# Performance work log

Measured on AMD Instinct MI355X. Metric: run time of the kernel, lower is better.

## Reference

```python
import jax, jax.numpy as jnp
import numpy as np

B, T, C = 2, 1024, 384
H, D = 4, 96            # heads, head_dim
BLK, NG = 16, 24        # HBS block size, num groups (NG*BLK == C)
SQ, PADM = 20, 400      # monarch grid dim, padded monarch dim
E, K, FF = 8, 2, 1536   # experts, top_k, expert hidden
EPS_LN = 1e-5


def _ln(x, g, b):
    m = jnp.mean(x, -1, keepdims=True)
    v = jnp.var(x, -1, keepdims=True)
    return (x - m) * jax.lax.rsqrt(v + EPS_LN) * g + b


def _hbs(x, pre_g, pre_b, blocks, wrow, wcol, alpha, bias):
    """HierarchicalBlockShuffleLayer: block mixing + flip + monarch, fp32."""
    orig = x.shape
    flat = _ln(x, pre_g, pre_b).astype(jnp.float32).reshape(-1, C)
    # block mixing: per-group 16x16 matmuls
    grouped = flat.reshape(-1, NG, BLK)
    y = jnp.einsum('ngb,gbc->ngc', grouped, blocks).reshape(-1, C)
    block_out = y[:, ::-1]  # torch.flip(dims=[-1])
    # monarch: pad to 400, view as 20x20 grid, left/right mix
    grid = jnp.pad(flat, ((0, 0), (0, PADM - C))).reshape(-1, SQ, SQ)
    z = jnp.einsum('nij,jk,lk->nil', grid, wcol, wrow)  # (x @ W_col) @ W_row.T
    mon = z.reshape(-1, PADM)[:, :C]
    out = block_out + alpha * mon + bias
    return out.reshape(orig)


def _rotary(t_len, d):
    inv = 1.0 / (10000.0 ** (jnp.arange(0, d, 2, dtype=jnp.float32) / d))
    fr = jnp.outer(jnp.arange(t_len, dtype=jnp.float32), inv)  # [T, d/2]
    emb = jnp.concatenate([fr, fr], -1)                        # [T, d]
    return jnp.cos(emb), jnp.sin(emb)


def _rotate_half(x):
    x1, x2 = x[..., : x.shape[-1] // 2], x[..., x.shape[-1] // 2:]
    return jnp.concatenate([-x2, x1], -1)


def _attention(xn, qkv_w, qkv_b, proj_pre_g, proj_pre_b, proj_blocks,
               proj_wrow, proj_wcol, proj_alpha, proj_bias,
               attn_norm_g, attn_norm_b, out_norm_g, out_norm_b, focus_gate):
    qkv = xn @ qkv_w + qkv_b  # [B,T,3C]
    q, k, v = jnp.split(qkv, 3, axis=-1)
    q = q.reshape(B, T, H, D).transpose(0, 2, 1, 3)  # bhtd
    k = k.reshape(B, T, H, D).transpose(0, 2, 1, 3)
    v = v.reshape(B, T, H, D).transpose(0, 2, 1, 3)
    cos, sin = _rotary(T, D)
    cos, sin = cos[None, None], sin[None, None]
    q = q * cos + _rotate_half(q) * sin
    k = k * cos + _rotate_half(k) * sin
    scale = 1.0 / jnp.sqrt(jnp.float32(D))
    # ---- linear attention branch (fp32, cumsum recurrence) ----
    Qp = jax.nn.elu(q * scale) + 1.0
    Kp = jax.nn.elu(k * scale) + 1.0
    KV = Kp[..., :, None] * v[..., None, :]          # bhtde
    KVc = jnp.cumsum(KV, axis=2)
    Kc = jnp.cumsum(Kp, axis=2)
    num = jnp.einsum('bhtd,bhtde->bhte', Qp, KVc)
    den = jnp.einsum('bhtd,bhtd->bht', Qp, Kc)[..., None]
    y_lin = num / (den + 1e-4)
    y_lin = _ln(y_lin, attn_norm_g, attn_norm_b)     # LN over head_dim
    # ---- sharp causal SDPA branch ----
    scores = jnp.einsum('bhtd,bhsd->bhts', q, k) * scale
    mask = jnp.tril(jnp.ones((T, T), dtype=bool))
    scores = jnp.where(mask, scores, -jnp.inf)
    y_sharp = jnp.einsum('bhts,bhsd->bhtd', jax.nn.softmax(scores, -1), v)
    # ---- gated combine ----
    a = jax.nn.sigmoid(focus_gate)
    y = a * y_sharp + (1.0 - a) * y_lin
    y = y.transpose(0, 2, 1, 3).reshape(B, T, C)
    y = _ln(y, out_norm_g, out_norm_b)
    return _hbs(y, proj_pre_g, proj_pre_b, proj_blocks, proj_wrow, proj_wcol,
                proj_alpha, proj_bias)


def _moe(xn, gate_w, w1, b1, w2, b2):
    xf = xn.reshape(-1, C)  # [N,C]
    logits = jnp.clip(xf @ gate_w, -20.0, 20.0)
    w, idx = jax.lax.top_k(logits, K)
    w = jax.nn.softmax(w, -1)
    # dense per-token expert weights [N,E] (same math as sparse dispatch, eval mode)
    wfull = jnp.sum(jax.nn.one_hot(idx, E, dtype=xf.dtype) * w[..., None], axis=1)
    h = jax.nn.gelu(jnp.einsum('nc,ech->neh', xf, w1) + b1, approximate=False)
    o = jnp.einsum('neh,ehc->nec', h, w2) + b2
    out = jnp.einsum('nec,ne->nc', o, wfull)
    return out.reshape(B, T, C)


def setup_inputs() -> dict:
    key = jax.random.key(0)
    ks = jax.random.split(key, 10)
    s = 0.02
    return {
        'x': jax.random.normal(ks[0], (B, T, C), jnp.float32),
        'ln1_g': jnp.ones((C,), jnp.float32), 'ln1_b': jnp.zeros((C,), jnp.float32),
        'ln2_g': jnp.ones((C,), jnp.float32), 'ln2_b': jnp.zeros((C,), jnp.float32),
        'qkv_w': jax.random.normal(ks[1], (C, 3 * C), jnp.float32) * s,
        'qkv_b': jnp.zeros((3 * C,), jnp.float32),
        'proj_pre_g': jnp.ones((C,), jnp.float32), 'proj_pre_b': jnp.zeros((C,), jnp.float32),
        'proj_blocks': jax.random.normal(ks[2], (NG, BLK, BLK), jnp.float32) * 0.125,
        'proj_wrow': jax.random.normal(ks[3], (SQ, SQ), jnp.float32) * 0.05,
        'proj_wcol': jax.random.normal(ks[4], (SQ, SQ), jnp.float32) * 0.05,
        'proj_alpha': jnp.zeros((), jnp.float32),
        'proj_bias': jnp.zeros((C,), jnp.float32),
        'attn_norm_g': jnp.ones((D,), jnp.float32), 'attn_norm_b': jnp.zeros((D,), jnp.float32),
        'out_norm_g': jnp.ones((C,), jnp.float32), 'out_norm_b': jnp.zeros((C,), jnp.float32),
        'focus_gate': jnp.zeros((), jnp.float32),
        'gate_w': jax.random.normal(ks[5], (C, E), jnp.float32) * s,
        'moe_w1': jax.random.normal(ks[6], (E, C, FF), jnp.float32) * s,
        'moe_b1': jnp.zeros((E, FF), jnp.float32),
        'moe_w2': jax.random.normal(ks[7], (E, FF, C), jnp.float32) * s,
        'moe_b2': jnp.zeros((E, C), jnp.float32),
    }


def reference(x, ln1_g, ln1_b, ln2_g, ln2_b, qkv_w, qkv_b,
              proj_pre_g, proj_pre_b, proj_blocks, proj_wrow, proj_wcol,
              proj_alpha, proj_bias, attn_norm_g, attn_norm_b,
              out_norm_g, out_norm_b, focus_gate, gate_w,
              moe_w1, moe_b1, moe_w2, moe_b2):
    h = x + _attention(_ln(x, ln1_g, ln1_b), qkv_w, qkv_b, proj_pre_g, proj_pre_b,
                       proj_blocks, proj_wrow, proj_wcol, proj_alpha, proj_bias,
                       attn_norm_g, attn_norm_b, out_norm_g, out_norm_b, focus_gate)
    out = h + _moe(_ln(h, ln2_g, ln2_b), gate_w, moe_w1, moe_b1, moe_w2, moe_b2)
    return out
```

## Files before the change

kernel.cpp:

```cpp
#include <hip/hip_runtime.h>
#include <math.h>

#define BB 2
#define TT 1024
#define CC 384
#define HH 4
#define DD 96
#define EE 8
#define FFD 1536
#define NROW (BB*TT)
#define QKVN (3*CC)
#define NSLOT (NROW*2)

typedef float f32x4 __attribute__((ext_vector_type(4)));
typedef short bf16x8 __attribute__((ext_vector_type(8)));

__device__ __forceinline__ float wredSum64(float v) {
#pragma unroll
  for (int o = 32; o > 0; o >>= 1) v += __shfl_xor(v, o, 64);
  return v;
}
__device__ __forceinline__ float rsum16(float v) {
#pragma unroll
  for (int o = 8; o > 0; o >>= 1) v += __shfl_xor(v, o, 16);
  return v;
}
__device__ __forceinline__ float rmax16(float v) {
#pragma unroll
  for (int o = 8; o > 0; o >>= 1) v = fmaxf(v, __shfl_xor(v, o, 16));
  return v;
}
__device__ __forceinline__ float dot4f(const float4 a, const float4 b) {
  return a.x*b.x + a.y*b.y + a.z*b.z + a.w*b.w;
}
__device__ __forceinline__ float blockRed128(float v, float* red) {
  v = wredSum64(v);
  const int w = threadIdx.x >> 6;
  if ((threadIdx.x & 63) == 0) red[w] = v;
  __syncthreads();
  float r = red[0] + red[1];
  __syncthreads();
  return r;
}
__device__ __forceinline__ float elup1(float x) {
  return x > 0.f ? x + 1.f : expf(x);
}
__device__ __forceinline__ unsigned short f2bf(float f) {
  unsigned int u = __float_as_uint(f);
  u = (u + 0x7FFFu + ((u >> 16) & 1u)) >> 16;
  return (unsigned short)u;
}

__global__ void zero_counts_kernel(int* counts) {
  if (threadIdx.x < EE) counts[threadIdx.x] = 0;
}

__global__ __launch_bounds__(256) void transconv_kernel(
    const float* __restrict__ src, unsigned short* __restrict__ dst,
    int K, int N) {
  src += (size_t)blockIdx.z * K * N;
  dst += (size_t)blockIdx.z * K * N;
  const int k0 = blockIdx.y * 32, n0 = blockIdx.x * 32;
  __shared__ float tile[32][33];
  const int t = threadIdx.x;
  const int ki = t >> 3, nj = (t & 7) * 4;
  const float4 v = *(const float4*)&src[(size_t)(k0 + ki) * N + n0 + nj];
  tile[ki][nj] = v.x; tile[ki][nj + 1] = v.y;
  tile[ki][nj + 2] = v.z; tile[ki][nj + 3] = v.w;
  __syncthreads();
  const int ni = t >> 3, kj = (t & 7) * 4;
  ushort4 o;
  o.x = f2bf(tile[kj][ni]);     o.y = f2bf(tile[kj + 1][ni]);
  o.z = f2bf(tile[kj + 2][ni]); o.w = f2bf(tile[kj + 3][ni]);
  *(ushort4*)&dst[(size_t)(n0 + ni) * K + k0 + kj] = o;
}

__global__ __launch_bounds__(64) void ln_row_kernel(
    const float* __restrict__ xin, const float* __restrict__ g,
    const float* __restrict__ b, float* __restrict__ xout) {
  const int row = blockIdx.x;
  const int lane = threadIdx.x;
  const size_t base = (size_t)row * CC;
  float v[6];
#pragma unroll
  for (int p = 0; p < 6; ++p) v[p] = xin[base + lane + 64 * p];
  float s = v[0] + v[1] + v[2] + v[3] + v[4] + v[5];
  s = wredSum64(s);
  const float mu = s * (1.f / CC);
  float sq = 0.f;
#pragma unroll
  for (int p = 0; p < 6; ++p) { float d = v[p] - mu; sq += d * d; }
  sq = wredSum64(sq);
  const float rinv = rsqrtf(sq * (1.f / CC) + 1e-5f);
#pragma unroll
  for (int p = 0; p < 6; ++p) {
    const int c = lane + 64 * p;
    xout[base + c] = (v[p] - mu) * rinv * g[c] + b[c];
  }
}

__global__ __launch_bounds__(256) void gemm_qkv_kernel(
    const float* __restrict__ A, const float* __restrict__ Bw,
    const float* __restrict__ bias, float* __restrict__ Cout) {
  const int N = QKVN, K = CC;
  const int n0 = blockIdx.x * 64, m0 = blockIdx.y * 64;
  __shared__ float As[16][68];
  __shared__ float Bs[16][64];
  const int tid = threadIdx.x, tx = tid & 15, ty = tid >> 4;
  const int akk = tid & 15, am = tid >> 4;
  const int bn = tid & 63, bk = tid >> 6;
  float acc[4][4] = {};
  for (int k0 = 0; k0 < K; k0 += 16) {
#pragma unroll
    for (int q = 0; q < 4; ++q) {
      As[akk][am + 16 * q] = A[(size_t)(m0 + am + 16 * q) * K + k0 + akk];
      Bs[bk + 4 * q][bn] = Bw[(size_t)(k0 + bk + 4 * q) * N + n0 + bn];
    }
    __syncthreads();
#pragma unroll
    for (int kk = 0; kk < 16; ++kk) {
      const float4 av = *(const float4*)&As[kk][ty * 4];
      const float4 bv = *(const float4*)&Bs[kk][tx * 4];
      const float aa[4] = {av.x, av.y, av.z, av.w};
      const float bb4[4] = {bv.x, bv.y, bv.z, bv.w};
#pragma unroll
      for (int i = 0; i < 4; ++i)
#pragma unroll
        for (int jj = 0; jj < 4; ++jj) acc[i][jj] += aa[i] * bb4[jj];
    }
    __syncthreads();
  }
#pragma unroll
  for (int i = 0; i < 4; ++i) {
    const int r = m0 + ty * 4 + i;
#pragma unroll
    for (int jj = 0; jj < 4; ++jj) {
      const int c = n0 + tx * 4 + jj;
      Cout[(size_t)r * N + c] = acc[i][jj] + bias[c];
    }
  }
}

__global__ __launch_bounds__(256) void rope_kernel(
    const float* __restrict__ qkv, float* __restrict__ qr, float* __restrict__ kr,
    float* __restrict__ qp, float* __restrict__ kp) {
  const int gid = blockIdx.x * 256 + threadIdx.x;
  const int i = gid % 48;
  const int t = (gid / 48) % TT;
  const int h = (gid / (48 * TT)) % HH;
  const int b = gid / (48 * TT * HH);
  const float inv = 1.0f / powf(10000.0f, (float)i * (1.0f / 48.0f));
  const float ang = (float)t * inv;
  float sn, cs;
  sincosf(ang, &sn, &cs);
  const float* row = qkv + ((size_t)(b * TT + t)) * QKVN + h * DD;
  const float q1 = row[i], q2 = row[i + 48];
  const float k1 = row[CC + i], k2 = row[CC + i + 48];
  const float qo1 = q1 * cs - q2 * sn, qo2 = q2 * cs + q1 * sn;
  const float ko1 = k1 * cs - k2 * sn, ko2 = k2 * cs + k1 * sn;
  const size_t ob = ((size_t)((b * HH + h) * TT + t)) * DD;
  qr[ob + i] = qo1; qr[ob + i + 48] = qo2;
  kr[ob + i] = ko1; kr[ob + i + 48] = ko2;
  const float scale = 0.10206207261596577f;
  qp[ob + i] = elup1(qo1 * scale); qp[ob + i + 48] = elup1(qo2 * scale);
  kp[ob + i] = elup1(ko1 * scale); kp[ob + i + 48] = elup1(ko2 * scale);
}

__global__ __launch_bounds__(256, 2) void attn_kernel(
    const float* __restrict__ qr, const float* __restrict__ kr,
    const float* __restrict__ qp, const float* __restrict__ kp,
    const float* __restrict__ qkv, const float* __restrict__ ang,
    const float* __restrict__ anb, const float* __restrict__ fgp,
    float* __restrict__ y_attn) {
  __shared__ float Qt[16][100];
  __shared__ float Qpt[16][100];
  __shared__ float Kt[32][100];
  __shared__ float Kpt[32][100];
  __shared__ float Vt[32][100];
  __shared__ float Ps[16][34];
  __shared__ float Pl[16][34];
  const int idx = blockIdx.x;
  const int qt = 63 - (idx >> 3);
  const int bh = idx & 7, b = bh >> 2, h = bh & 3;
  const int tid = threadIdx.x, j = tid & 15, rg = tid >> 4;
  const float a = 1.f / (1.f + expf(-fgp[0]));
  const int t0 = qt << 4;
  const int t = t0 + rg;
  const size_t qbase = ((size_t)bh * TT + t0) * DD;
#pragma unroll
  for (int p = 0; p < 6; ++p) {
    const int i = tid + 256 * p, r = i / 96, d = i - r * 96;
    Qt[r][d] = qr[qbase + i];
    Qpt[r][d] = qp[qbase + i];
  }
  float accS[6] = {}, accN[6] = {};
  float mrow = -1e30f, lrow = 0.f, den = 0.f;
  const int nc = (qt >> 1) + 1;
  __syncthreads();
  for (int c = 0; c < nc; ++c) {
    const int s0 = c << 5;
    const float* vb = qkv + ((size_t)(b * TT + s0)) * QKVN + 2 * CC + h * DD;
    const size_t kb = ((size_t)bh * TT + s0) * DD;
#pragma unroll
    for (int p = 0; p < 12; ++p) {
      const int i = tid + 256 * p, s = i / 96, d = i - s * 96;
      Kt[s][d] = kr[kb + i];
      Kpt[s][d] = kp[kb + i];
      Vt[s][d] = vb[(size_t)s * QKVN + d];
    }
    __syncthreads();
    float ds0 = 0.f, ds1 = 0.f, dl0 = 0.f, dl1 = 0.f;
#pragma unroll
    for (int dd = 0; dd < 96; dd += 4) {
      const float4 qa = *(const float4*)&Qt[rg][dd];
      const float4 ka = *(const float4*)&Kt[j][dd];
      const float4 k2 = *(const float4*)&Kt[j + 16][dd];
      ds0 += dot4f(qa, ka); ds1 += dot4f(qa, k2);
      const float4 pa = *(const float4*)&Qpt[rg][dd];
      const float4 fa = *(const float4*)&Kpt[j][dd];
      const float4 f2 = *(const float4*)&Kpt[j + 16][dd];
      dl0 += dot4f(pa, fa); dl1 += dot4f(pa, f2);
    }
    const float scale = 0.10206207261596577f;
    float sc0 = ds0 * scale, sc1 = ds1 * scale;
    if (c == nc - 1) {
      if (s0 + j > t)      { sc0 = -1e30f; dl0 = 0.f; }
      if (s0 + j + 16 > t) { sc1 = -1e30f; dl1 = 0.f; }
    }
    const float cm = rmax16(fmaxf(sc0, sc1));
    const float mn = fmaxf(mrow, cm);
    const float sf = expf(mrow - mn);
    const float p0 = expf(sc0 - mn), p1 = expf(sc1 - mn);
    lrow = lrow * sf + rsum16(p0 + p1);
    mrow = mn;
    den += rsum16(dl0 + dl1);
#pragma unroll
    for (int u = 0; u < 6; ++u) accS[u] *= sf;
    Ps[rg][j] = p0; Ps[rg][j + 16] = p1;
    Pl[rg][j] = dl0; Pl[rg][j + 16] = dl1;
    __syncthreads();
    const int c0 = j * 6;
#pragma unroll
    for (int s = 0; s < 32; s += 2) {
      const float2 pA = *(const float2*)&Ps[rg][s];
      const float2 lA = *(const float2*)&Pl[rg][s];
      const float* v0p = &Vt[s][c0];
      const float* v1p = v0p + 100;
      float va[6], vb2[6];
      *(float2*)&va[0] = *(const float2*)(v0p);
      *(float2*)&va[2] = *(const float2*)(v0p + 2);
      *(float2*)&va[4] = *(const float2*)(v0p + 4);
      *(float2*)&vb2[0] = *(const float2*)(v1p);
      *(float2*)&vb2[2] = *(const float2*)(v1p + 2);
      *(float2*)&vb2[4] = *(const float2*)(v1p + 4);
#pragma unroll
      for (int u = 0; u < 6; ++u) {
        accS[u] += pA.x * va[u] + pA.y * vb2[u];
        accN[u] += lA.x * va[u] + lA.y * vb2[u];
      }
    }
    __syncthreads();
  }
  const float invl = 1.0f / lrow;
  const float dinv = 1.0f / (den + 1e-4f);
  float yl[6];
  float s1 = 0.f;
#pragma unroll
  for (int u = 0; u < 6; ++u) { yl[u] = accN[u] * dinv; s1 += yl[u]; }
  s1 = rsum16(s1);
  const float mu = s1 * (1.f / DD);
  float s2 = 0.f;
#pragma unroll
  for (int u = 0; u < 6; ++u) { const float d = yl[u] - mu; s2 += d * d; }
  s2 = rsum16(s2);
  const float rr = rsqrtf(s2 * (1.f / DD) + 1e-5f);
  const size_t ob = ((size_t)(b * TT + t)) * CC + h * DD + j * 6;
#pragma unroll
  for (int u = 0; u < 6; ++u) {
    const float ylin = (yl[u] - mu) * rr * ang[j * 6 + u] + anb[j * 6 + u];
    const float ys = accS[u] * invl;
    y_attn[ob + u] = a * ys + (1.f - a) * ylin;
  }
}

__global__ __launch_bounds__(128) void hbs_kernel(
    const float* __restrict__ y_attn, const float* __restrict__ x,
    const float* __restrict__ outg, const float* __restrict__ outb,
    const float* __restrict__ preg, const float* __restrict__ preb,
    const float* __restrict__ blocks, const float* __restrict__ wrow,
    const float* __restrict__ wcol, const float* __restrict__ alphap,
    const float* __restrict__ biasv, const float* __restrict__ ln2g,
    const float* __restrict__ ln2b, const float* __restrict__ gatew,
    float* __restrict__ hout, unsigned short* __restrict__ xn2,
    int* __restrict__ tok_idx, float* __restrict__ tok_w, int* __restrict__ counts) {
  __shared__ float flatS[CC];
  __shared__ float ybuf[CC];
  __shared__ float xbuf[CC];
  __shared__ float tmp[400];
  __shared__ float red[2];
  __shared__ float logit[EE];
  const int row = blockIdx.x, tid = threadIdx.x;
  const size_t base = (size_t)row * CC;
  float v[3];
#pragma unroll
  for (int p = 0; p < 3; ++p) v[p] = y_attn[base + tid + 128 * p];
  float s = blockRed128(v[0] + v[1] + v[2], red);
  float mu = s * (1.f / CC);
  float sq = 0.f;
#pragma unroll
  for (int p = 0; p < 3; ++p) { const float d = v[p] - mu; sq += d * d; }
  sq = blockRed128(sq, red);
  float rin = rsqrtf(sq * (1.f / CC) + 1e-5f);
  float w[3];
#pragma unroll
  for (int p = 0; p < 3; ++p) {
    const int c = tid + 128 * p;
    w[p] = (v[p] - mu) * rin * outg[c] + outb[c];
  }
  s = blockRed128(w[0] + w[1] + w[2], red);
  mu = s * (1.f / CC);
  sq = 0.f;
#pragma unroll
  for (int p = 0; p < 3; ++p) { const float d = w[p] - mu; sq += d * d; }
  sq = blockRed128(sq, red);
  rin = rsqrtf(sq * (1.f / CC) + 1e-5f);
#pragma unroll
  for (int p = 0; p < 3; ++p) {
    const int c = tid + 128 * p;
    flatS[c] = (w[p] - mu) * rin * preg[c] + preb[c];
  }
  __syncthreads();
#pragma unroll
  for (int p = 0; p < 3; ++p) {
    const int o = tid + 128 * p;
    const int g = o >> 4, cc = o & 15;
    const float* bp = blocks + g * 256 + cc;
    const float* fp = flatS + g * 16;
    float acc = 0.f;
#pragma unroll
    for (int bb = 0; bb < 16; ++bb) acc += fp[bb] * bp[bb * 16];
    ybuf[o] = acc;
  }
#pragma unroll
  for (int p = 0; p < 4; ++p) {
    const int o = tid + 128 * p;
    if (o < 400) {
      const int i = o / 20, k = o - i * 20;
      float acc = 0.f;
#pragma unroll
      for (int jj = 0; jj < 20; ++jj) {
        const int src = i * 20 + jj;
        const float gv = (src < CC) ? flatS[src] : 0.f;
        acc += gv * wcol[jj * 20 + k];
      }
      tmp[o] = acc;
    }
  }
  __syncthreads();
  const float alpha = alphap[0];
  float hr[3];
#pragma unroll
  for (int p = 0; p < 3; ++p) {
    const int o = tid + 128 * p;
    const int i = o / 20, ll = o - i * 20;
    float mon = 0.f;
#pragma unroll
    for (int k = 0; k < 20; ++k) mon += tmp[i * 20 + k] * wrow[ll * 20 + k];
    const float hb = ybuf[383 - o] + alpha * mon + biasv[o];
    const float hv = x[base + o] + hb;
    hout[base + o] = hv;
    hr[p] = hv;
  }
  s = blockRed128(hr[0] + hr[1] + hr[2], red);
  mu = s * (1.f / CC);
  sq = 0.f;
#pragma unroll
  for (int p = 0; p < 3; ++p) { const float d = hr[p] - mu; sq += d * d; }
  sq = blockRed128(sq, red);
  rin = rsqrtf(sq * (1.f / CC) + 1e-5f);
#pragma unroll
  for (int p = 0; p < 3; ++p) {
    const int c = tid + 128 * p;
    const float xv = (hr[p] - mu) * rin * ln2g[c] + ln2b[c];
    xn2[base + c] = f2bf(xv);
    xbuf[c] = xv;
  }
  __syncthreads();
  const int e = tid >> 4, jj = tid & 15;
  float part = 0.f;
  for (int c = jj; c < CC; c += 16) part += xbuf[c] * gatew[c * EE + e];
  part = rsum16(part);
  if (jj == 0) logit[e] = fminf(20.f, fmaxf(-20.f, part));
  __syncthreads();
  if (tid == 0) {
    float lg[EE];
#pragma unroll
    for (int ee = 0; ee < EE; ++ee) lg[ee] = logit[ee];
    int i0 = 0; float v0 = lg[0];
#pragma unroll
    for (int ee = 1; ee < EE; ++ee) if (lg[ee] > v0) { v0 = lg[ee]; i0 = ee; }
    int i1 = -1; float v1 = -1e30f;
#pragma unroll
    for (int ee = 0; ee < EE; ++ee)
      if (ee != i0 && lg[ee] > v1) { v1 = lg[ee]; i1 = ee; }
    const float e1 = expf(v1 - v0);
    const float w0 = 1.f / (1.f + e1), w1 = e1 / (1.f + e1);
    tok_idx[2 * row] = i0; tok_idx[2 * row + 1] = i1;
    tok_w[2 * row] = w0; tok_w[2 * row + 1] = w1;
    atomicAdd(&counts[i0], 1);
    atomicAdd(&counts[i1], 1);
  }
}

__global__ void r_offsets_kernel(const int* __restrict__ counts, int* offsets, int* cursor) {
  if (threadIdx.x == 0) {
    int acc = 0;
    for (int e = 0; e < EE; ++e) { offsets[e] = acc; cursor[e] = acc; acc += counts[e]; }
  }
}
__global__ __launch_bounds__(256) void r_scatter_kernel(
    const int* __restrict__ tok_idx, const float* __restrict__ tok_w,
    int* cursor, int* __restrict__ perm, float* __restrict__ slotw,
    int* __restrict__ dest) {
  const int n = blockIdx.x * 256 + threadIdx.x;
  if (n >= NROW) return;
#pragma unroll
  for (int k = 0; k < 2; ++k) {
    const int e = tok_idx[2 * n + k];
    const int pos = atomicAdd(&cursor[e], 1);
    perm[pos] = n;
    slotw[pos] = tok_w[2 * n + k];
    dest[pos] = 2 * n + k;
  }
}


__global__ __launch_bounds__(256) void gemm_moe1_kernel(
    const unsigned short* __restrict__ xn2b, const unsigned short* __restrict__ w1t,
    const float* __restrict__ b1, const int* __restrict__ perm,
    const int* __restrict__ offsets, const int* __restrict__ counts,
    unsigned short* __restrict__ hbuf) {
  const int e = blockIdx.z;
  const int cnt = counts[e];
  const int m0 = blockIdx.y * 64;
  if (m0 >= cnt) return;
  const int n0 = blockIdx.x * 64;
  const int off = offsets[e];
  __shared__ __align__(16) short As[64][40];
  __shared__ __align__(16) short Bs[64][40];
  const int t = threadIdx.x;
  const int srow = t >> 2, sko = (t & 3) * 8;
  const int w = t >> 6, lane = t & 63, lm = lane & 15, kg8 = (lane >> 4) * 8;
  const int wr = (w >> 1) * 32, wc = (w & 1) * 32;
  const int sm = m0 + srow;
  const int grow = perm[off + (sm < cnt ? sm : cnt - 1)];
  const unsigned short* aro = xn2b + (size_t)grow * CC;
  const unsigned short* bro = w1t + ((size_t)e * FFD + n0 + srow) * CC;
  f32x4 acc[2][2] = {};
  for (int k0 = 0; k0 < CC; k0 += 32) {
    *(float4*)&As[srow][sko] = *(const float4*)(aro + k0 + sko);
    *(float4*)&Bs[srow][sko] = *(const float4*)(bro + k0 + sko);
    __syncthreads();
    const bf16x8 a0 = *(const bf16x8*)&As[wr + lm][kg8];
    const bf16x8 a1 = *(const bf16x8*)&As[wr + lm + 16][kg8];
    const bf16x8 b0 = *(const bf16x8*)&Bs[wc + lm][kg8];
    const bf16x8 b1v = *(const bf16x8*)&Bs[wc + lm + 16][kg8];
    acc[0][0] = __builtin_amdgcn_mfma_f32_16x16x32_bf16(a0, b0, acc[0][0], 0, 0, 0);
    acc[0][1] = __builtin_amdgcn_mfma_f32_16x16x32_bf16(a0, b1v, acc[0][1], 0, 0, 0);
    acc[1][0] = __builtin_amdgcn_mfma_f32_16x16x32_bf16(a1, b0, acc[1][0], 0, 0, 0);
    acc[1][1] = __builtin_amdgcn_mfma_f32_16x16x32_bf16(a1, b1v, acc[1][1], 0, 0, 0);
    __syncthreads();
  }
#pragma unroll
  for (int mi = 0; mi < 2; ++mi)
#pragma unroll
    for (int r = 0; r < 4; ++r) {
      const int m = m0 + wr + mi * 16 + (lane >> 4) * 4 + r;
      if (m < cnt) {
#pragma unroll
        for (int ni = 0; ni < 2; ++ni) {
          const int c = n0 + wc + ni * 16 + lm;
          const float tv = acc[mi][ni][r] + b1[e * FFD + c];
          const float gel = 0.5f * tv * (1.0f + erff(tv * 0.70710678118654752f));
          hbuf[(size_t)(off + m) * FFD + c] = f2bf(gel);
        }
      }
    }
}

__global__ __launch_bounds__(256) void gemm_moe2_kernel(
    const unsigned short* __restrict__ hbuf, const unsigned short* __restrict__ w2t,
    const float* __restrict__ b2, const int* __restrict__ offsets,
    const int* __restrict__ counts, const int* __restrict__ dest,
    const float* __restrict__ slotw, float* __restrict__ so) {
  const int e = blockIdx.z;
  const int cnt = counts[e];
  const int m0 = blockIdx.y * 64;
  if (m0 >= cnt) return;
  const int n0 = blockIdx.x * 64;
  const int off = offsets[e];
  __shared__ __align__(16) short As[64][40];
  __shared__ __align__(16) short Bs[64][40];
  const int t = threadIdx.x;
  const int srow = t >> 2, sko = (t & 3) * 8;
  const int w = t >> 6, lane = t & 63, lm = lane & 15, kg8 = (lane >> 4) * 8;
  const int wr = (w >> 1) * 32, wc = (w & 1) * 32;
  const int sm = m0 + srow;
  const unsigned short* aro = hbuf + (size_t)(off + (sm < cnt ? sm : cnt - 1)) * FFD;
  const unsigned short* bro = w2t + ((size_t)e * CC + n0 + srow) * FFD;
  f32x4 acc[2][2] = {};
  for (int k0 = 0; k0 < FFD; k0 += 32) {
    *(float4*)&As[srow][sko] = *(const float4*)(aro + k0 + sko);
    *(float4*)&Bs[srow][sko] = *(const float4*)(bro + k0 + sko);
    __syncthreads();
    const bf16x8 a0 = *(const bf16x8*)&As[wr + lm][kg8];
    const bf16x8 a1 = *(const bf16x8*)&As[wr + lm + 16][kg8];
    const bf16x8 b0 = *(const bf16x8*)&Bs[wc + lm][kg8];
    const bf16x8 b1v = *(const bf16x8*)&Bs[wc + lm + 16][kg8];
    acc[0][0] = __builtin_amdgcn_mfma_f32_16x16x32_bf16(a0, b0, acc[0][0], 0, 0, 0);
    acc[0][1] = __builtin_amdgcn_mfma_f32_16x16x32_bf16(a0, b1v, acc[0][1], 0, 0, 0);
    acc[1][0] = __builtin_amdgcn_mfma_f32_16x16x32_bf16(a1, b0, acc[1][0], 0, 0, 0);
    acc[1][1] = __builtin_amdgcn_mfma_f32_16x16x32_bf16(a1, b1v, acc[1][1], 0, 0, 0);
    __syncthreads();
  }
#pragma unroll
  for (int mi = 0; mi < 2; ++mi)
#pragma unroll
    for (int r = 0; r < 4; ++r) {
      const int m = m0 + wr + mi * 16 + (lane >> 4) * 4 + r;
      if (m < cnt) {
        const int sIdx = off + m;
        const int dd = dest[sIdx];
        const float wv = slotw[sIdx];
#pragma unroll
        for (int ni = 0; ni < 2; ++ni) {
          const int c = n0 + wc + ni * 16 + lm;
          so[(size_t)dd * CC + c] = wv * (acc[mi][ni][r] + b2[e * CC + c]);
        }
      }
    }
}

__global__ __launch_bounds__(256) void final_kernel(
    const float* __restrict__ h, const float* __restrict__ so,
    float* __restrict__ out) {
  const int i = blockIdx.x * 256 + threadIdx.x;
  const int n = i / 96, c = i - n * 96;
  const float4* h4 = (const float4*)h;
  const float4* s4 = (const float4*)so;
  float4* o4 = (float4*)out;
  const float4 a = h4[i];
  const float4 b0 = s4[(size_t)n * 192 + c];
  const float4 b1 = s4[(size_t)n * 192 + 96 + c];
  o4[i] = make_float4(a.x + b0.x + b1.x, a.y + b0.y + b1.y,
                      a.z + b0.z + b1.z, a.w + b0.w + b1.w);
}

extern "C" void kernel_launch(void* const* d_in, const int* in_sizes, int n_in,
                              void* d_out, int out_size, void* d_ws, size_t ws_size,
                              hipStream_t stream) {
  const float* x          = (const float*)d_in[0];
  const float* ln1_g      = (const float*)d_in[1];
  const float* ln1_b      = (const float*)d_in[2];
  const float* ln2_g      = (const float*)d_in[3];
  const float* ln2_b      = (const float*)d_in[4];
  const float* qkv_w      = (const float*)d_in[5];
  const float* qkv_b      = (const float*)d_in[6];
  const float* pre_g      = (const float*)d_in[7];
  const float* pre_b      = (const float*)d_in[8];
  const float* blocks     = (const float*)d_in[9];
  const float* wrow       = (const float*)d_in[10];
  const float* wcol       = (const float*)d_in[11];
  const float* alpha      = (const float*)d_in[12];
  const float* biasv      = (const float*)d_in[13];
  const float* ang        = (const float*)d_in[14];
  const float* anb        = (const float*)d_in[15];
  const float* outg       = (const float*)d_in[16];
  const float* outb       = (const float*)d_in[17];
  const float* fg         = (const float*)d_in[18];
  const float* gatew      = (const float*)d_in[19];
  const float* w1         = (const float*)d_in[20];
  const float* b1         = (const float*)d_in[21];
  const float* w2         = (const float*)d_in[22];
  const float* b2         = (const float*)d_in[23];
  float* out = (float*)d_out;

  char* ws = (char*)d_ws;
  constexpr size_t SZ_ROWC  = (size_t)NROW * CC * 4;
  constexpr size_t SZ_QKV   = (size_t)NROW * QKVN * 4;
  constexpr size_t SZ_HEAD  = (size_t)BB * HH * TT * DD * 4;
  constexpr size_t SZ_HMID  = (size_t)NSLOT * FFD * 4;
  constexpr size_t OFF_A    = 0;
  constexpr size_t OFF_B    = OFF_A + SZ_ROWC;
  constexpr size_t OFF_QR   = OFF_B + SZ_QKV;
  constexpr size_t OFF_KR   = OFF_QR + SZ_HEAD;
  constexpr size_t OFF_QP   = OFF_KR + SZ_HEAD;
  constexpr size_t OFF_KP   = OFF_QP + SZ_HEAD;
  constexpr size_t OFF_HB   = OFF_B + SZ_HMID;
  constexpr size_t OFF_XN2  = OFF_HB + SZ_ROWC;
  constexpr size_t OFF_SO   = OFF_XN2 + SZ_ROWC;
  constexpr size_t OFF_TI   = OFF_SO + (size_t)NSLOT * CC * 4;
  constexpr size_t OFF_TW   = OFF_TI + NSLOT * 4;
  constexpr size_t OFF_PERM = OFF_TW + NSLOT * 4;
  constexpr size_t OFF_SW   = OFF_PERM + NSLOT * 4;
  constexpr size_t OFF_DEST = OFF_SW + NSLOT * 4;
  constexpr size_t OFF_CNT  = OFF_DEST + NSLOT * 4;
  constexpr size_t OFF_OFFS = OFF_CNT + 256;
  constexpr size_t OFF_CUR  = OFF_OFFS + 256;
  constexpr size_t OFF_W1T  = OFF_CUR + 256;
  constexpr size_t OFF_W2T  = OFF_W1T + (size_t)EE * FFD * CC * 2;

  float* xn    = (float*)(ws + OFF_A);
  float* yat   = (float*)(ws + OFF_A);
  float* qkv   = (float*)(ws + OFF_B);
  float* qr    = (float*)(ws + OFF_QR);
  float* kr    = (float*)(ws + OFF_KR);
  float* qp    = (float*)(ws + OFF_QP);
  float* kp    = (float*)(ws + OFF_KP);
  unsigned short* hmid = (unsigned short*)(ws + OFF_B);
  float* hbufr = (float*)(ws + OFF_HB);
  unsigned short* xn2b = (unsigned short*)(ws + OFF_XN2);
  float* so    = (float*)(ws + OFF_SO);
  int*   tok_idx = (int*)(ws + OFF_TI);
  float* tok_w   = (float*)(ws + OFF_TW);
  int*   perm    = (int*)(ws + OFF_PERM);
  float* slotw   = (float*)(ws + OFF_SW);
  int*   dest    = (int*)(ws + OFF_DEST);
  int*   counts  = (int*)(ws + OFF_CNT);
  int*   offsets = (int*)(ws + OFF_OFFS);
  int*   cursor  = (int*)(ws + OFF_CUR);
  unsigned short* w1T  = (unsigned short*)(ws + OFF_W1T);
  unsigned short* w2T  = (unsigned short*)(ws + OFF_W2T);

  zero_counts_kernel<<<1, 64, 0, stream>>>(counts);
  transconv_kernel<<<dim3(FFD / 32, CC / 32, EE), 256, 0, stream>>>(w1, w1T, CC, FFD);
  transconv_kernel<<<dim3(CC / 32, FFD / 32, EE), 256, 0, stream>>>(w2, w2T, FFD, CC);
  ln_row_kernel<<<NROW, 64, 0, stream>>>(x, ln1_g, ln1_b, xn);
  gemm_qkv_kernel<<<dim3(QKVN / 64, NROW / 64), 256, 0, stream>>>(xn, qkv_w, qkv_b, qkv);
  rope_kernel<<<(BB * HH * TT * 48) / 256, 256, 0, stream>>>(qkv, qr, kr, qp, kp);
  attn_kernel<<<dim3(512), 256, 0, stream>>>(qr, kr, qp, kp, qkv, ang, anb, fg, yat);
  hbs_kernel<<<NROW, 128, 0, stream>>>(yat, x, outg, outb, pre_g, pre_b, blocks,
                                       wrow, wcol, alpha, biasv, ln2_g, ln2_b,
                                       gatew, hbufr, xn2b, tok_idx, tok_w, counts);
  r_offsets_kernel<<<1, 64, 0, stream>>>(counts, offsets, cursor);
  r_scatter_kernel<<<NROW / 256, 256, 0, stream>>>(tok_idx, tok_w, cursor, perm, slotw, dest);
  gemm_moe1_kernel<<<dim3(FFD / 64, NROW / 64, EE), 256, 0, stream>>>(
      xn2b, w1T, b1, perm, offsets, counts, hmid);
  gemm_moe2_kernel<<<dim3(CC / 64, NROW / 64, EE), 256, 0, stream>>>(
      hmid, w2T, b2, offsets, counts, dest, slotw, so);
  final_kernel<<<(NROW * CC / 4) / 256, 256, 0, stream>>>(hbufr, so, out);
}
```

Measured before the change: 483.3 us.

## Compute two query rows per thread in attention and vectorize tile loads

The attention kernel drops to 128 threads per block, and each thread now handles two query rows. This reuses every K/Kp/V shared-memory read across both rows and halves the redundant LDS traffic. Global-to-shared loads for Q, K and V are switched to float4, and the QKV GEMM tile loads are also vectorized to float4. The costs are higher register pressure per thread and fewer threads per block, which may lower latency hiding.

```diff
diff --git a/kernel.cpp b/kernel.cpp
--- a/kernel.cpp
+++ b/kernel.cpp
@@ -107,15 +107,15 @@
   __shared__ float As[16][68];
   __shared__ float Bs[16][64];
   const int tid = threadIdx.x, tx = tid & 15, ty = tid >> 4;
-  const int akk = tid & 15, am = tid >> 4;
-  const int bn = tid & 63, bk = tid >> 6;
+  const int am = tid >> 2, akq = (tid & 3) * 4;
+  const int bkk = tid >> 4, bn4 = (tid & 15) * 4;
   float acc[4][4] = {};
   for (int k0 = 0; k0 < K; k0 += 16) {
-#pragma unroll
-    for (int q = 0; q < 4; ++q) {
-      As[akk][am + 16 * q] = A[(size_t)(m0 + am + 16 * q) * K + k0 + akk];
-      Bs[bk + 4 * q][bn] = Bw[(size_t)(k0 + bk + 4 * q) * N + n0 + bn];
-    }
+    const float4 av4 = *(const float4*)&A[(size_t)(m0 + am) * K + k0 + akq];
+    As[akq + 0][am] = av4.x; As[akq + 1][am] = av4.y;
+    As[akq + 2][am] = av4.z; As[akq + 3][am] = av4.w;
+    *(float4*)&Bs[bkk][bn4] =
+        *(const float4*)&Bw[(size_t)(k0 + bkk) * N + n0 + bn4];
     __syncthreads();
 #pragma unroll
     for (int kk = 0; kk < 16; ++kk) {
@@ -166,7 +166,7 @@
   kp[ob + i] = elup1(ko1 * scale); kp[ob + i + 48] = elup1(ko2 * scale);
 }
 
-__global__ __launch_bounds__(256, 2) void attn_kernel(
+__global__ __launch_bounds__(128, 3) void attn_kernel(
     const float* __restrict__ qr, const float* __restrict__ kr,
     const float* __restrict__ qp, const float* __restrict__ kp,
     const float* __restrict__ qkv, const float* __restrict__ ang,
@@ -182,19 +182,20 @@
   const int idx = blockIdx.x;
   const int qt = 63 - (idx >> 3);
   const int bh = idx & 7, b = bh >> 2, h = bh & 3;
-  const int tid = threadIdx.x, j = tid & 15, rg = tid >> 4;
+  const int tid = threadIdx.x;
+  const int j = tid & 15;
+  const int r = tid >> 4;
   const float a = 1.f / (1.f + expf(-fgp[0]));
   const int t0 = qt << 4;
-  const int t = t0 + rg;
   const size_t qbase = ((size_t)bh * TT + t0) * DD;
 #pragma unroll
-  for (int p = 0; p < 6; ++p) {
-    const int i = tid + 256 * p, r = i / 96, d = i - r * 96;
-    Qt[r][d] = qr[qbase + i];
-    Qpt[r][d] = qp[qbase + i];
-  }
-  float accS[6] = {}, accN[6] = {};
-  float mrow = -1e30f, lrow = 0.f, den = 0.f;
+  for (int p = 0; p < 3; ++p) {
+    const int i4 = tid + 128 * p, s = i4 / 24, d4 = (i4 % 24) * 4;
+    *(float4*)&Qt[s][d4]  = *(const float4*)&qr[qbase + i4 * 4];
+    *(float4*)&Qpt[s][d4] = *(const float4*)&qp[qbase + i4 * 4];
+  }
+  float accS[2][6] = {}, accN[2][6] = {};
+  float mrow[2] = {-1e30f, -1e30f}, lrow[2] = {0.f, 0.f}, den[2] = {0.f, 0.f};
   const int nc = (qt >> 1) + 1;
   __syncthreads();
   for (int c = 0; c < nc; ++c) {
@@ -202,48 +203,73 @@
     const float* vb = qkv + ((size_t)(b * TT + s0)) * QKVN + 2 * CC + h * DD;
     const size_t kb = ((size_t)bh * TT + s0) * DD;
 #pragma unroll
-    for (int p = 0; p < 12; ++p) {
-      const int i = tid + 256 * p, s = i / 96, d = i - s * 96;
-      Kt[s][d] = kr[kb + i];
-      Kpt[s][d] = kp[kb + i];
-      Vt[s][d] = vb[(size_t)s * QKVN + d];
-    }
-    __syncthreads();
-    float ds0 = 0.f, ds1 = 0.f, dl0 = 0.f, dl1 = 0.f;
+    for (int p = 0; p < 6; ++p) {
+      const int i4 = tid + 128 * p, s = i4 / 24, d4 = (i4 % 24) * 4;
+      *(float4*)&Kt[s][d4]  = *(const float4*)&kr[kb + i4 * 4];
+      *(float4*)&Kpt[s][d4] = *(const float4*)&kp[kb + i4 * 4];
+      *(float4*)&Vt[s][d4]  = *(const float4*)&vb[(size_t)s * QKVN + d4];
+    }
+    __syncthreads();
+    float ds00 = 0, ds01 = 0, ds10 = 0, ds11 = 0;
+    float dl00 = 0, dl01 = 0, dl10 = 0, dl11 = 0;
 #pragma unroll
     for (int dd = 0; dd < 96; dd += 4) {
-      const float4 qa = *(const float4*)&Qt[rg][dd];
+      const float4 qa = *(const float4*)&Qt[r][dd];
+      const float4 qb = *(const float4*)&Qt[r + 8][dd];
       const float4 ka = *(const float4*)&Kt[j][dd];
       const float4 k2 = *(const float4*)&Kt[j + 16][dd];
-      ds0 += dot4f(qa, ka); ds1 += dot4f(qa, k2);
-      const float4 pa = *(const float4*)&Qpt[rg][dd];
+      ds00 += dot4f(qa, ka); ds01 += dot4f(qa, k2);
+      ds10 += dot4f(qb, ka); ds11 += dot4f(qb, k2);
+      const float4 pa = *(const float4*)&Qpt[r][dd];
+      const float4 pb = *(const float4*)&Qpt[r + 8][dd];
       const float4 fa = *(const float4*)&Kpt[j][dd];
       const float4 f2 = *(const float4*)&Kpt[j + 16][dd];
-      dl0 += dot4f(pa, fa); dl1 += dot4f(pa, f2);
+      dl00 += dot4f(pa, fa); dl01 += dot4f(pa, f2);
+      dl10 += dot4f(pb, fa); dl11 += dot4f(pb, f2);
     }
     const float scale = 0.10206207261596577f;
-    float sc0 = ds0 * scale, sc1 = ds1 * scale;
+    float sc00 = ds00 * scale, sc01 = ds01 * scale;
+    float sc10 = ds10 * scale, sc11 = ds11 * scale;
     if (c == nc - 1) {
-      if (s0 + j > t)      { sc0 = -1e30f; dl0 = 0.f; }
-      if (s0 + j + 16 > t) { sc1 = -1e30f; dl1 = 0.f; }
-    }
-    const float cm = rmax16(fmaxf(sc0, sc1));
-    const float mn = fmaxf(mrow, cm);
-    const float sf = expf(mrow - mn);
-    const float p0 = expf(sc0 - mn), p1 = expf(sc1 - mn);
-    lrow = lrow * sf + rsum16(p0 + p1);
-    mrow = mn;
-    den += rsum16(dl0 + dl1);
-#pragma unroll
-    for (int u = 0; u < 6; ++u) accS[u] *= sf;
-    Ps[rg][j] = p0; Ps[rg][j + 16] = p1;
-    Pl[rg][j] = dl0; Pl[rg][j + 16] = dl1;
+      if (s0 + j > t0 + r)          { sc00 = -1e30f; dl00 = 0.f; }
+      if (s0 + j + 16 > t0 + r)     { sc01 = -1e30f; dl01 = 0.f; }
+      if (s0 + j > t0 + r + 8)      { sc10 = -1e30f; dl10 = 0.f; }
+      if (s0 + j + 16 > t0 + r + 8) { sc11 = -1e30f; dl11 = 0.f; }
+    }
+    {
+      const float cm = rmax16(fmaxf(sc00, sc01));
+      const float mn = fmaxf(mrow[0], cm);
+      const float sf = expf(mrow[0] - mn);
+      const float p0 = expf(sc00 - mn), p1 = expf(sc01 - mn);
+      lrow[0] = lrow[0] * sf + rsum16(p0 + p1);
+      mrow[0] = mn;
+      den[0] += rsum16(dl00 + dl01);
+#pragma unroll
+      for (int u = 0; u < 6; ++u) accS[0][u] *= sf;
+      Ps[r][j] = p0; Ps[r][j + 16] = p1;
+      Pl[r][j] = dl00; Pl[r][j + 16] = dl01;
+    }
+    {
+      const float cm = rmax16(fmaxf(sc10, sc11));
+      const float mn = fmaxf(mrow[1], cm);
+      const float sf = expf(mrow[1] - mn);
+      const float p0 = expf(sc10 - mn), p1 = expf(sc11 - mn);
+      lrow[1] = lrow[1] * sf + rsum16(p0 + p1);
+      mrow[1] = mn;
+      den[1] += rsum16(dl10 + dl11);
+#pragma unroll
+      for (int u = 0; u < 6; ++u) accS[1][u] *= sf;
+      Ps[r + 8][j] = p0; Ps[r + 8][j + 16] = p1;
+      Pl[r + 8][j] = dl10; Pl[r + 8][j + 16] = dl11;
+    }
     __syncthreads();
     const int c0 = j * 6;
 #pragma unroll
     for (int s = 0; s < 32; s += 2) {
-      const float2 pA = *(const float2*)&Ps[rg][s];
-      const float2 lA = *(const float2*)&Pl[rg][s];
+      const float2 pA = *(const float2*)&Ps[r][s];
+      const float2 pB = *(const float2*)&Ps[r + 8][s];
+      const float2 lA = *(const float2*)&Pl[r][s];
+      const float2 lB = *(const float2*)&Pl[r + 8][s];
       const float* v0p = &Vt[s][c0];
       const float* v1p = v0p + 100;
       float va[6], vb2[6];
@@ -255,31 +281,37 @@
       *(float2*)&vb2[4] = *(const float2*)(v1p + 4);
 #pragma unroll
       for (int u = 0; u < 6; ++u) {
-        accS[u] += pA.x * va[u] + pA.y * vb2[u];
-        accN[u] += lA.x * va[u] + lA.y * vb2[u];
+        accS[0][u] += pA.x * va[u] + pA.y * vb2[u];
+        accS[1][u] += pB.x * va[u] + pB.y * vb2[u];
+        accN[0][u] += lA.x * va[u] + lA.y * vb2[u];
+        accN[1][u] += lB.x * va[u] + lB.y * vb2[u];
       }
     }
     __syncthreads();
   }
-  const float invl = 1.0f / lrow;
-  const float dinv = 1.0f / (den + 1e-4f);
-  float yl[6];
-  float s1 = 0.f;
-#pragma unroll
-  for (int u = 0; u < 6; ++u) { yl[u] = accN[u] * dinv; s1 += yl[u]; }
-  s1 = rsum16(s1);
-  const float mu = s1 * (1.f / DD);
-  float s2 = 0.f;
-#pragma unroll
-  for (int u = 0; u < 6; ++u) { const float d = yl[u] - mu; s2 += d * d; }
-  s2 = rsum16(s2);
-  const float rr = rsqrtf(s2 * (1.f / DD) + 1e-5f);
-  const size_t ob = ((size_t)(b * TT + t)) * CC + h * DD + j * 6;
-#pragma unroll
-  for (int u = 0; u < 6; ++u) {
-    const float ylin = (yl[u] - mu) * rr * ang[j * 6 + u] + anb[j * 6 + u];
-    const float ys = accS[u] * invl;
-    y_attn[ob + u] = a * ys + (1.f - a) * ylin;
+#pragma unroll
+  for (int ri = 0; ri < 2; ++ri) {
+    const int t = t0 + r + 8 * ri;
+    const float invl = 1.0f / lrow[ri];
+    const float dinv = 1.0f / (den[ri] + 1e-4f);
+    float yl[6];
+    float s1 = 0.f;
+#pragma unroll
+    for (int u = 0; u < 6; ++u) { yl[u] = accN[ri][u] * dinv; s1 += yl[u]; }
+    s1 = rsum16(s1);
+    const float mu = s1 * (1.f / DD);
+    float s2 = 0.f;
+#pragma unroll
+    for (int u = 0; u < 6; ++u) { const float d = yl[u] - mu; s2 += d * d; }
+    s2 = rsum16(s2);
+    const float rr = rsqrtf(s2 * (1.f / DD) + 1e-5f);
+    const size_t ob = ((size_t)(b * TT + t)) * CC + h * DD + j * 6;
+#pragma unroll
+    for (int u = 0; u < 6; ++u) {
+      const float ylin = (yl[u] - mu) * rr * ang[j * 6 + u] + anb[j * 6 + u];
+      const float ys = accS[ri][u] * invl;
+      y_attn[ob + u] = a * ys + (1.f - a) * ylin;
+    }
   }
 }
 
@@ -638,7 +670,7 @@
   ln_row_kernel<<<NROW, 64, 0, stream>>>(x, ln1_g, ln1_b, xn);
   gemm_qkv_kernel<<<dim3(QKVN / 64, NROW / 64), 256, 0, stream>>>(xn, qkv_w, qkv_b, qkv);
   rope_kernel<<<(BB * HH * TT * 48) / 256, 256, 0, stream>>>(qkv, qr, kr, qp, kp);
-  attn_kernel<<<dim3(512), 256, 0, stream>>>(qr, kr, qp, kp, qkv, ang, anb, fg, yat);
+  attn_kernel<<<dim3(512), 128, 0, stream>>>(qr, kr, qp, kp, qkv, ang, anb, fg, yat);
   hbs_kernel<<<NROW, 128, 0, stream>>>(yat, x, outg, outb, pre_g, pre_b, blocks,
                                        wrow, wcol, alpha, biasv, ln2_g, ln2_b,
                                        gatew, hbufr, xn2b, tok_idx, tok_w, counts);
```

After: 510.5 us. 1.06x slower.
